# Kernel tuning notes

Hardware: AMD Instinct MI355X
Metric: run time of the kernel (lower is better)

The kernel has to match this reference:

```python
import jax, jax.numpy as jnp
import numpy as np

B, IN, OUT, TDIM, YDIM = 4096, 48, 64, 128, 64
HID = OUT * OUT  # 4096, Y_layer hidden/output width


def setup_inputs() -> dict:
    key = jax.random.key(0)
    ks = jax.random.split(key, 9)
    x = jax.random.normal(ks[0], (B, IN, IN), dtype=jnp.float32)
    # symmetrize so input is SPD-like (module assumes SPD inputs)
    x = 0.5 * (x + jnp.swapaxes(x, 1, 2))
    t = jax.random.normal(ks[1], (B, TDIM), dtype=jnp.float32)
    Y = jax.random.normal(ks[2], (B, YDIM), dtype=jnp.float32)
    # Stiefel (orthogonal) weight [input_size(=OUT after increase), output_size]
    W, _ = jnp.linalg.qr(jax.random.normal(ks[3], (OUT, OUT), dtype=jnp.float32))
    # Y_layer MLP params: Linear(YDIM,HID) -> SiLU -> Linear(HID,HID)
    Y_W1 = jax.random.normal(ks[4], (YDIM, HID), dtype=jnp.float32) / np.sqrt(YDIM)
    Y_b1 = jnp.zeros((HID,), dtype=jnp.float32)
    Y_W2 = jax.random.normal(ks[5], (HID, HID), dtype=jnp.float32) / np.sqrt(HID)
    Y_b2 = jnp.zeros((HID,), dtype=jnp.float32)
    return {"input": x, "t": t, "Y": Y, "W": W,
            "Y_W1": Y_W1, "Y_b1": Y_b1, "Y_W2": Y_W2, "Y_b2": Y_b2}


def reference(input, t, Y, W, Y_W1, Y_b1, Y_W2, Y_b2):
    # Y_layer MLP -> per-sample transform emb_Y [B, OUT, OUT]
    h = jax.nn.silu(Y @ Y_W1 + Y_b1)
    emb_Y = (h @ Y_W2 + Y_b2).reshape(B, OUT, OUT)
    # SPDIncreaseDim: embed input in top-left of OUTxOUT, ones on padded diagonal
    pad = OUT - IN
    xp = jnp.pad(input, ((0, 0), (0, pad), (0, pad)))
    add_diag = jnp.concatenate([jnp.zeros(IN, input.dtype), jnp.ones(pad, input.dtype)])
    xp = xp + jnp.diag(add_diag)[None]
    # congruence with Stiefel weight: W^T X W
    out = jnp.einsum('ji,bjk,kl->bil', W, xp, W)
    # congruence with MLP-generated weight: emb_Y X emb_Y^T
    out = jnp.einsum('bij,bjk,blk->bil', emb_Y, out, emb_Y)
    return out
```

## Files before the change

### kernel.cpp

```cpp
#include <hip/hip_runtime.h>
#include <hip/hip_bf16.h>

typedef __bf16 bf16;
typedef __bf16 bf16x8 __attribute__((ext_vector_type(8)));
typedef float floatx4 __attribute__((ext_vector_type(4)));

#define MFMA16(a, b, c) __builtin_amdgcn_mfma_f32_16x16x32_bf16((a), (b), (c), 0, 0, 0)

__device__ inline void gload_lds16(const void* g, void* l) {
    __builtin_amdgcn_global_load_lds((__attribute__((address_space(1))) void*)g,
                                     (__attribute__((address_space(3))) void*)l, 16, 0, 0);
}

__global__ __launch_bounds__(256) void prep_fused(
    const float* __restrict__ W2,
    const float* __restrict__ W,
    const float* __restrict__ b2,
    const float* __restrict__ Y,
    const float* __restrict__ W1,
    const float* __restrict__ b1,
    bf16* __restrict__ W2fT,
    float* __restrict__ b2f,
    bf16* __restrict__ h)
{
    __shared__ __align__(16) char smem[45056];
    int t = threadIdx.x, bid = blockIdx.x;
    int w = t >> 6, l = t & 63;
    int lm = l & 15, q2 = l >> 4, q8 = q2 * 8;

    if (bid < 2048) {
        int pt = bid & 31, i = bid >> 5;
        bf16* sW = (bf16*)smem;
        bf16* sA = sW + 64 * 72;
        bf16* sT = sA + 128 * 72;
        int p0 = pt * 128;

#pragma unroll
        for (int kk = 0; kk < 16; kk++) {
            int idx = t + 256 * kk;
            sW[(idx >> 6) * 72 + (idx & 63)] = (bf16)W[idx];
        }
        {
            const float* src = W2 + (size_t)p0 * 4096 + i * 64;
#pragma unroll
            for (int kk = 0; kk < 8; kk++) {
                int c = t + 256 * kk;
                int row = c >> 4, j4 = (c & 15) * 4;
                float4 v = *(const float4*)(src + (size_t)row * 4096 + j4);
                bf16 tmp[4] = {(bf16)v.x, (bf16)v.y, (bf16)v.z, (bf16)v.w};
                *(uint2*)(sA + row * 72 + j4) = *(const uint2*)tmp;
            }
        }
        __syncthreads();

        floatx4 acc[2][4] = {};
#pragma unroll
        for (int kc = 0; kc < 2; kc++) {
            bf16x8 a0 = *(const bf16x8*)(sA + (w * 32 + lm) * 72 + kc * 32 + q8);
            bf16x8 a1 = *(const bf16x8*)(sA + (w * 32 + 16 + lm) * 72 + kc * 32 + q8);
#pragma unroll
            for (int jn = 0; jn < 4; jn++) {
                bf16x8 bf_ = *(const bf16x8*)(sW + (jn * 16 + lm) * 72 + kc * 32 + q8);
                acc[0][jn] = MFMA16(a0, bf_, acc[0][jn]);
                acc[1][jn] = MFMA16(a1, bf_, acc[1][jn]);
            }
        }
#pragma unroll
        for (int im = 0; im < 2; im++)
#pragma unroll
            for (int jn = 0; jn < 4; jn++) {
                int pr = w * 32 + im * 16 + q2 * 4;
                int lc = jn * 16 + lm;
                union { bf16 h4[4]; uint2 u; } pk;
#pragma unroll
                for (int r = 0; r < 4; r++) pk.h4[r] = (bf16)acc[im][jn][r];
                *(uint2*)(sT + lc * 136 + pr) = pk.u;
            }
        __syncthreads();
#pragma unroll
        for (int kk = 0; kk < 4; kk++) {
            int c = t + 256 * kk;
            int row = c >> 4, off = (c & 15) * 8;
            uint4 v = *(const uint4*)(sT + row * 136 + off);
            *(uint4*)(W2fT + (size_t)(i * 64 + row) * 4096 + p0 + off) = v;
        }
        return;
    }

    if (bid < 2112) {
        int i = bid - 2048;
        if (t < 64) {
            float acc = 0.f;
            const float* b2r = b2 + i * 64;
            const float* wr_ = W + t * 64;
#pragma unroll
            for (int j = 0; j < 64; j++) acc = fmaf(b2r[j], wr_[j], acc);
            b2f[i * 64 + t] = acc;
        }
        return;
    }

    {
        int q = bid - 2112;
        int m0 = (q >> 5) * 128, n0 = (q & 31) * 128;
        bf16* sY = (bf16*)smem;
        bf16* sWT = sY + 128 * 72;

#pragma unroll
        for (int kk = 0; kk < 8; kk++) {
            int c = t + 256 * kk;
            int row = c >> 4, c4 = (c & 15) * 4;
            float4 v = *(const float4*)(Y + (size_t)(m0 + row) * 64 + c4);
            bf16 tmp[4] = {(bf16)v.x, (bf16)v.y, (bf16)v.z, (bf16)v.w};
            *(uint2*)(sY + row * 72 + c4) = *(const uint2*)tmp;
        }
#pragma unroll
        for (int kk = 0; kk < 8; kk++) {
            int c = t + 256 * kk;
            int k = c >> 5, j4 = (c & 31) * 4;
            float4 v = *(const float4*)(W1 + (size_t)k * 4096 + n0 + j4);
            sWT[(j4 + 0) * 72 + k] = (bf16)v.x;
            sWT[(j4 + 1) * 72 + k] = (bf16)v.y;
            sWT[(j4 + 2) * 72 + k] = (bf16)v.z;
            sWT[(j4 + 3) * 72 + k] = (bf16)v.w;
        }
        __syncthreads();

        int wn = (w & 1) * 64, wm = (w >> 1) * 64;
        floatx4 acc[4][4] = {};
#pragma unroll
        for (int kc = 0; kc < 2; kc++) {
            bf16x8 af[4], bfr[4];
#pragma unroll
            for (int i = 0; i < 4; i++)
                af[i] = *(const bf16x8*)(sWT + (wn + i * 16 + lm) * 72 + kc * 32 + q8);
#pragma unroll
            for (int j = 0; j < 4; j++)
                bfr[j] = *(const bf16x8*)(sY + (wm + j * 16 + lm) * 72 + kc * 32 + q8);
#pragma unroll
            for (int i = 0; i < 4; i++)
#pragma unroll
                for (int j = 0; j < 4; j++)
                    acc[i][j] = MFMA16(af[i], bfr[j], acc[i][j]);
        }
#pragma unroll
        for (int i = 0; i < 4; i++) {
            int nb = n0 + wn + i * 16 + q2 * 4;
            float4 bv = *(const float4*)(b1 + nb);
            float bb[4] = {bv.x, bv.y, bv.z, bv.w};
#pragma unroll
            for (int j = 0; j < 4; j++) {
                int m = m0 + wm + j * 16 + lm;
                union { bf16 h4[4]; uint2 u; } pk;
#pragma unroll
                for (int r = 0; r < 4; r++) {
                    float v = acc[i][j][r] + bb[r];
                    v = v / (1.f + __expf(-v));
                    pk.h4[r] = (bf16)v;
                }
                *(uint2*)(h + (size_t)m * 4096 + nb) = pk.u;
            }
        }
    }
}

#define GT 128
#define GK 32
__global__ __launch_bounds__(256, 4) void gemm_bt_bias(
    const bf16* __restrict__ A, const bf16* __restrict__ BT,
    const float* __restrict__ bias, bf16* __restrict__ C,
    int M, int N, int K)
{
    __shared__ bf16 sA[2][GT * GK];
    __shared__ bf16 sB[2][GT * GK];
    int t = threadIdx.x, w = t >> 6, l = t & 63;

    int bid = blockIdx.x;
    int xcd = bid & 7, local = bid >> 3;
    int mt = xcd * 4 + (local & 3);
    int nt = local >> 2;
    int m0 = mt * GT, n0 = nt * GT;

    int lm = l & 15;
    int q2 = l >> 4;
    int soff = ((q2 - (l & 3)) & 3) * 8;
    int wr = (w >> 1) * 64, wc = (w & 1) * 64;

    int rowA = (w * 64 + l) >> 2;
    int ko = (((l & 3) + rowA) & 3) * 8;
    const bf16* pa = A + (size_t)(m0 + rowA) * K + ko;
    const bf16* pb = BT + (size_t)(n0 + rowA) * K + ko;
    const int base0 = (w * 64) * 8, base1 = (w * 64 + 256) * 8;

    floatx4 acc[4][4] = {};

    auto issue = [&](int buf, const bf16* a, const bf16* b) {
        gload_lds16(a, &sA[buf][base0]);
        gload_lds16(a + (size_t)64 * K, &sA[buf][base1]);
        gload_lds16(b, &sB[buf][base0]);
        gload_lds16(b + (size_t)64 * K, &sB[buf][base1]);
    };

    const int KT = K / GK;
    issue(0, pa, pb);
    pa += GK; pb += GK;
    __syncthreads();

    for (int kt = 0; kt < KT; ++kt) {
        int cur = kt & 1;
        if (kt + 1 < KT) {
            issue(cur ^ 1, pa, pb);
            pa += GK; pb += GK;
        }
        const bf16* LA = sA[cur];
        const bf16* LB = sB[cur];
        bf16x8 af[4], bfr[4];
#pragma unroll
        for (int i = 0; i < 4; i++)
            af[i] = *(const bf16x8*)(LA + (wr + i * 16 + lm) * GK + soff);
#pragma unroll
        for (int j = 0; j < 4; j++)
            bfr[j] = *(const bf16x8*)(LB + (wc + j * 16 + lm) * GK + soff);
#pragma unroll
        for (int i = 0; i < 4; i++)
#pragma unroll
            for (int j = 0; j < 4; j++)
                acc[i][j] = MFMA16(af[i], bfr[j], acc[i][j]);
        __syncthreads();
    }

#pragma unroll
    for (int i = 0; i < 4; i++) {
        int r0 = m0 + wr + i * 16 + (l >> 4) * 4;
#pragma unroll
        for (int j = 0; j < 4; j++) {
            int cc = n0 + wc + j * 16 + lm;
            float bb = bias[cc];
#pragma unroll
            for (int r = 0; r < 4; r++)
                C[(size_t)(r0 + r) * N + cc] = (bf16)(acc[i][j][r] + bb);
        }
    }
}

#define ST 72
__global__ __launch_bounds__(256) void batched_congruence(
    const float* __restrict__ x,
    const bf16* __restrict__ F,
    float* __restrict__ out)
{
    __shared__ bf16 sX[64 * ST], sF[64 * ST], sT[64 * ST];
    int t = threadIdx.x, w = t >> 6, l = t & 63;
    int b = blockIdx.x;
    int lm = l & 15, q2 = l >> 4, q8 = q2 * 8;
    int r0 = (w >> 1) * 32, c0 = (w & 1) * 32;

    const float4* xb = (const float4*)(x + (size_t)b * 2304);
    float4 v0 = xb[t];
    float4 v1 = xb[t + 256];
    float4 v2 = (t < 64) ? xb[t + 512] : make_float4(0.f, 0.f, 0.f, 0.f);

    {
        const uint4* gf = (const uint4*)(F + (size_t)b * 4096);
#pragma unroll
        for (int kk = 0; kk < 2; kk++) {
            int c = t + 256 * kk;
            *(uint4*)(sF + (c >> 3) * ST + (c & 7) * 8) = gf[c];
        }
    }
    {
        unsigned* sx32 = (unsigned*)sX;
#pragma unroll
        for (int kk = 0; kk < 4; kk++) {
            int idx = t + 256 * kk;
            if (idx < 384) {
                int r = idx >> 3, d = 24 + (idx & 7);
                sx32[r * 36 + d] = 0u;
            } else if (idx < 896) {
                int k2 = idx - 384;
                int r = 48 + (k2 >> 5), d = k2 & 31;
                unsigned val = 0u;
                if (d == (r >> 1)) val = (r & 1) ? 0x3F800000u : 0x00003F80u;
                sx32[r * 36 + d] = val;
            }
        }
    }
    {
        int c = t;
        bf16 p4[4];
        p4[0] = (bf16)v0.x; p4[1] = (bf16)v0.y; p4[2] = (bf16)v0.z; p4[3] = (bf16)v0.w;
        *(uint2*)(sX + (c / 12) * ST + (c % 12) * 4) = *(const uint2*)p4;
        c = t + 256;
        p4[0] = (bf16)v1.x; p4[1] = (bf16)v1.y; p4[2] = (bf16)v1.z; p4[3] = (bf16)v1.w;
        *(uint2*)(sX + (c / 12) * ST + (c % 12) * 4) = *(const uint2*)p4;
        if (t < 64) {
            c = t + 512;
            p4[0] = (bf16)v2.x; p4[1] = (bf16)v2.y; p4[2] = (bf16)v2.z; p4[3] = (bf16)v2.w;
            *(uint2*)(sX + (c / 12) * ST + (c % 12) * 4) = *(const uint2*)p4;
        }
    }
    __syncthreads();

    auto mm = [&](const bf16* PA, const bf16* PB, floatx4 acc[2][2]) {
#pragma unroll
        for (int kc = 0; kc < 2; kc++) {
            bf16x8 a0 = *(const bf16x8*)(PA + (r0 + lm) * ST + kc * 32 + q8);
            bf16x8 a1 = *(const bf16x8*)(PA + (r0 + 16 + lm) * ST + kc * 32 + q8);
            bf16x8 b0 = *(const bf16x8*)(PB + (c0 + lm) * ST + kc * 32 + q8);
            bf16x8 b1 = *(const bf16x8*)(PB + (c0 + 16 + lm) * ST + kc * 32 + q8);
            acc[0][0] = MFMA16(a0, b0, acc[0][0]);
            acc[0][1] = MFMA16(a0, b1, acc[0][1]);
            acc[1][0] = MFMA16(a1, b0, acc[1][0]);
            acc[1][1] = MFMA16(a1, b1, acc[1][1]);
        }
    };

    floatx4 z = {0.f, 0.f, 0.f, 0.f};
    {
        floatx4 acc[2][2] = {{z, z}, {z, z}};
        mm(sX, sF, acc);
#pragma unroll
        for (int i = 0; i < 2; i++)
#pragma unroll
            for (int j = 0; j < 2; j++) {
                int R = r0 + i * 16 + q2 * 4;
                int Cc = c0 + j * 16 + lm;
                union { bf16 h4[4]; uint2 u; } pk;
#pragma unroll
                for (int r = 0; r < 4; r++) pk.h4[r] = (bf16)acc[i][j][r];
                *(uint2*)(sT + Cc * ST + R) = pk.u;
            }
    }
    __syncthreads();
    {
        floatx4 acc[2][2] = {{z, z}, {z, z}};
        mm(sT, sF, acc);
        float* ob = out + (size_t)b * 4096;
#pragma unroll
        for (int i = 0; i < 2; i++)
#pragma unroll
            for (int j = 0; j < 2; j++) {
                int R = r0 + i * 16 + q2 * 4;
                int Cc = c0 + j * 16 + lm;
#pragma unroll
                for (int r = 0; r < 4; r++)
                    out[(size_t)b * 4096 + (size_t)(R + r) * 64 + Cc] = acc[i][j][r];
            }
        (void)ob;
    }
}

extern "C" void kernel_launch(void* const* d_in, const int* in_sizes, int n_in,
                              void* d_out, int out_size, void* d_ws, size_t ws_size,
                              hipStream_t stream) {
    const float* x  = (const float*)d_in[0];
    const float* Y  = (const float*)d_in[2];
    const float* W  = (const float*)d_in[3];
    const float* W1 = (const float*)d_in[4];
    const float* b1 = (const float*)d_in[5];
    const float* W2 = (const float*)d_in[6];
    const float* b2 = (const float*)d_in[7];
    float* out = (float*)d_out;

    const size_t NN = (size_t)4096 * 4096;
    bf16* h    = (bf16*)d_ws;
    bf16* W2fT = h + NN;
    bf16* emb  = W2fT + NN;
    float* b2f = (float*)d_out;

    prep_fused<<<3136, 256, 0, stream>>>(W2, W, b2, Y, W1, b1, W2fT, b2f, h);
    gemm_bt_bias<<<1024, 256, 0, stream>>>(h, W2fT, b2f, emb, 4096, 4096, 4096);
    batched_congruence<<<4096, 256, 0, stream>>>(x, emb, out);
}
```

Before: 338.9 us.

## Rewrite main GEMM with 256x256 tiles, 4-stage LDS pipeline and 8 waves

Replaces the 128x128 tile, double-buffered GEMM with a 256x256 tile computed by 512-thread blocks, each wave holding a 128x64 accumulator. Loads go through a 4-slot direct-to-LDS ring with explicit vmcnt waits, XOR-swizzled LDS layout, interleaved MFMA and LDS reads, and s_setprio around the math. The aim is more data reuse per global load and better overlap of memory with MFMA in the dominant 4096^3 GEMM. In exchange it uses 128KB of LDS and more registers, leaves 256 blocks for 256 CUs (one wave of work), and depends on hand-managed barrier and waitcnt ordering being correct.

```diff
diff --git a/kernel.cpp b/kernel.cpp
--- a/kernel.cpp
+++ b/kernel.cpp
@@ -164,77 +164,87 @@
     }
 }
 
-#define GT 128
-#define GK 32
-__global__ __launch_bounds__(256, 4) void gemm_bt_bias(
+__global__ __launch_bounds__(512, 2) void gemm_bt_bias(
     const bf16* __restrict__ A, const bf16* __restrict__ BT,
     const float* __restrict__ bias, bf16* __restrict__ C,
     int M, int N, int K)
 {
-    __shared__ bf16 sA[2][GT * GK];
-    __shared__ bf16 sB[2][GT * GK];
+    __shared__ __align__(16) char lds[131072];
+
     int t = threadIdx.x, w = t >> 6, l = t & 63;
+    int lm = l & 15, q2 = l >> 4;
+    int wm = w >> 2, wn = w & 3;
 
     int bid = blockIdx.x;
-    int xcd = bid & 7, local = bid >> 3;
-    int mt = xcd * 4 + (local & 3);
-    int nt = local >> 2;
-    int m0 = mt * GT, n0 = nt * GT;
-
-    int lm = l & 15;
-    int q2 = l >> 4;
-    int soff = ((q2 - (l & 3)) & 3) * 8;
-    int wr = (w >> 1) * 64, wc = (w & 1) * 64;
-
-    int rowA = (w * 64 + l) >> 2;
-    int ko = (((l & 3) + rowA) & 3) * 8;
-    const bf16* pa = A + (size_t)(m0 + rowA) * K + ko;
-    const bf16* pb = BT + (size_t)(n0 + rowA) * K + ko;
-    const int base0 = (w * 64) * 8, base1 = (w * 64 + 256) * 8;
-
-    floatx4 acc[4][4] = {};
-
-    auto issue = [&](int buf, const bf16* a, const bf16* b) {
-        gload_lds16(a, &sA[buf][base0]);
-        gload_lds16(a + (size_t)64 * K, &sA[buf][base1]);
-        gload_lds16(b, &sB[buf][base0]);
-        gload_lds16(b + (size_t)64 * K, &sB[buf][base1]);
+    int wg = (bid & 7) * 32 + (bid >> 3);
+    int m0 = (wg >> 4) * 256, n0 = (wg & 15) * 256;
+
+    int c1 = t + 512;
+    int ks0 = ((t & 3) ^ ((t >> 3) & 3)) * 8;
+    int ks1 = ((c1 & 3) ^ ((c1 >> 3) & 3)) * 8;
+    const bf16* gA0 = A + (size_t)(m0 + (t >> 2)) * K + ks0;
+    const bf16* gA1 = A + (size_t)(m0 + (c1 >> 2)) * K + ks1;
+    const bf16* gB0 = BT + (size_t)(n0 + (t >> 2)) * K + ks0;
+    const bf16* gB1 = BT + (size_t)(n0 + (c1 >> 2)) * K + ks1;
+    const int dst0 = (w * 64) * 16, dst1 = (512 + w * 64) * 16;
+
+    auto issue = [&](int slot) {
+        char* slab = lds + slot * 32768;
+        gload_lds16(gA0, slab + dst0);
+        gload_lds16(gA1, slab + dst1);
+        gload_lds16(gB0, slab + 16384 + dst0);
+        gload_lds16(gB1, slab + 16384 + dst1);
+        gA0 += 32; gA1 += 32; gB0 += 32; gB1 += 32;
     };
 
-    const int KT = K / GK;
-    issue(0, pa, pb);
-    pa += GK; pb += GK;
-    __syncthreads();
-
-    for (int kt = 0; kt < KT; ++kt) {
-        int cur = kt & 1;
-        if (kt + 1 < KT) {
-            issue(cur ^ 1, pa, pb);
-            pa += GK; pb += GK;
-        }
-        const bf16* LA = sA[cur];
-        const bf16* LB = sB[cur];
-        bf16x8 af[4], bfr[4];
+    const int qp16 = (q2 ^ ((lm >> 1) & 3)) * 16;
+    const int aoff = (wm * 128 + lm) * 64 + qp16;
+    const int boff = 16384 + (wn * 64 + lm) * 64 + qp16;
+
+    floatx4 acc[8][4] = {};
+
+    auto body = [&](int kt, bool doIssue) {
+        __builtin_amdgcn_s_barrier();
+        __builtin_amdgcn_sched_barrier(0);
+        asm volatile("" ::: "memory");
+        if (doIssue) issue((kt + 3) & 3);
+        const char* slab = lds + (kt & 3) * 32768;
+        bf16x8 av[8], bv[4];
+#pragma unroll
+        for (int j = 0; j < 4; j++) bv[j] = *(const bf16x8*)(slab + boff + j * 1024);
+#pragma unroll
+        for (int i = 0; i < 4; i++) av[i] = *(const bf16x8*)(slab + aoff + i * 1024);
+        __builtin_amdgcn_s_setprio(1);
 #pragma unroll
         for (int i = 0; i < 4; i++)
-            af[i] = *(const bf16x8*)(LA + (wr + i * 16 + lm) * GK + soff);
-#pragma unroll
-        for (int j = 0; j < 4; j++)
-            bfr[j] = *(const bf16x8*)(LB + (wc + j * 16 + lm) * GK + soff);
-#pragma unroll
-        for (int i = 0; i < 4; i++)
-#pragma unroll
-            for (int j = 0; j < 4; j++)
-                acc[i][j] = MFMA16(af[i], bfr[j], acc[i][j]);
-        __syncthreads();
-    }
-
-#pragma unroll
-    for (int i = 0; i < 4; i++) {
-        int r0 = m0 + wr + i * 16 + (l >> 4) * 4;
+#pragma unroll
+            for (int j = 0; j < 4; j++) acc[i][j] = MFMA16(av[i], bv[j], acc[i][j]);
+#pragma unroll
+        for (int i = 4; i < 8; i++) av[i] = *(const bf16x8*)(slab + aoff + i * 1024);
+#pragma unroll
+        for (int i = 4; i < 8; i++)
+#pragma unroll
+            for (int j = 0; j < 4; j++) acc[i][j] = MFMA16(av[i], bv[j], acc[i][j]);
+        __builtin_amdgcn_s_setprio(0);
+    };
+
+    issue(0); issue(1); issue(2);
+    const int KT = K >> 5;
+    for (int kt = 0; kt < KT - 2; ++kt) {
+        asm volatile("s_waitcnt vmcnt(8)" ::: "memory");
+        body(kt, kt < KT - 3);
+    }
+    asm volatile("s_waitcnt vmcnt(4)" ::: "memory");
+    body(KT - 2, false);
+    asm volatile("s_waitcnt vmcnt(0)" ::: "memory");
+    body(KT - 1, false);
+
+#pragma unroll
+    for (int i = 0; i < 8; i++) {
+        int r0 = m0 + wm * 128 + i * 16 + q2 * 4;
 #pragma unroll
         for (int j = 0; j < 4; j++) {
-            int cc = n0 + wc + j * 16 + lm;
+            int cc = n0 + wn * 64 + j * 16 + lm;
             float bb = bias[cc];
 #pragma unroll
             for (int r = 0; r < 4; r++)
@@ -335,7 +345,6 @@
     {
         floatx4 acc[2][2] = {{z, z}, {z, z}};
         mm(sT, sF, acc);
-        float* ob = out + (size_t)b * 4096;
 #pragma unroll
         for (int i = 0; i < 2; i++)
 #pragma unroll
@@ -346,7 +355,6 @@
                 for (int r = 0; r < 4; r++)
                     out[(size_t)b * 4096 + (size_t)(R + r) * 64 + Cc] = acc[i][j][r];
             }
-        (void)ob;
     }
 }
 
@@ -369,6 +377,6 @@
     float* b2f = (float*)d_out;
 
     prep_fused<<<3136, 256, 0, stream>>>(W2, W, b2, Y, W1, b1, W2fT, b2f, h);
-    gemm_bt_bias<<<1024, 256, 0, stream>>>(h, W2fT, b2f, emb, 4096, 4096, 4096);
+    gemm_bt_bias<<<256, 512, 0, stream>>>(h, W2fT, b2f, emb, 4096, 4096, 4096);
     batched_congruence<<<4096, 256, 0, stream>>>(x, emb, out);
 }
```

Result: faster. 303.1 us (-10.6%).
